# Kernel optimization log

Measured on AMD Instinct MI355X. Metric: run time of the kernel, lower is better.

## Reference

```python
import jax, jax.numpy as jnp
import numpy as np

N, E, D, C = 100000, 640000, 128, 4


def setup_inputs() -> dict:
    key = jax.random.key(0)
    ks = jax.random.split(key, 8)
    s = 1.0 / np.sqrt(D)
    return {
        "x": jax.random.normal(ks[0], (N, D), jnp.float32),
        "edge_index": jax.random.randint(ks[1], (2, E), 0, N),
        "edge_attr": jax.random.normal(ks[2], (E, D), jnp.float32),
        "masks": jax.random.uniform(ks[3], (C, N), jnp.float32),
        "W1": jax.random.normal(ks[4], (C, D, D), jnp.float32) * s,
        "b1": jnp.zeros((C, D), jnp.float32),
        "W2": jax.random.normal(ks[5], (C, D, D), jnp.float32) * s,
        "b2": jnp.zeros((C, D), jnp.float32),
        "eps": jnp.zeros((C,), jnp.float32),
        "gamma": jnp.ones((C, D), jnp.float32),
        "beta": jnp.zeros((C, D), jnp.float32),
        "run_mean": jnp.zeros((C, D), jnp.float32),
        "run_var": jnp.ones((C, D), jnp.float32),
    }


def reference(x, edge_index, edge_attr, masks, W1, b1, W2, b2, eps, gamma, beta, run_mean, run_var):
    BN_EPS = 1e-5
    src, dst = edge_index[0], edge_index[1]
    x_in = x
    for c in range(C):
        # GINEConv: sum_{j->i} relu(x_j + e_ij), then (1+eps)*x_i + agg -> MLP
        msg = jax.nn.relu(x[src] + edge_attr)                      # [E, D]
        agg = jax.ops.segment_sum(msg, dst, num_segments=x.shape[0])
        h = (1.0 + eps[c]) * x + agg
        h = jax.nn.relu(h @ W1[c] + b1[c]) @ W2[c] + b2[c]
        # masked sublayer residual
        x = masks[c][:, None] * h + x
        # BatchNorm1d (eval mode, running stats)
        x = (x - run_mean[c]) * jax.lax.rsqrt(run_var[c] + BN_EPS) * gamma[c] + beta[c]
    # final relu (dropout is identity in eval) + outer residual
    return x_in + jax.nn.relu(x)
```

## Files before the change

### kernel.cpp

```cpp
#include <hip/hip_runtime.h>
#include <cstddef>

#define D 128
#define CHUNK 1024
#define BM 64
#define LDSH 136

typedef __attribute__((ext_vector_type(8))) short s16x8;
typedef __attribute__((ext_vector_type(8))) unsigned short u16x8;
typedef __attribute__((ext_vector_type(4))) float f32x4;
typedef __attribute__((ext_vector_type(2))) float f32x2;

__device__ __forceinline__ unsigned short f2bf(float f) {
  unsigned u = __builtin_bit_cast(unsigned, f);
  u += 0x7FFFu + ((u >> 16) & 1u);
  return (unsigned short)(u >> 16);
}
__device__ __forceinline__ float bf2f(unsigned short h) {
  unsigned u = ((unsigned)h) << 16;
  return __builtin_bit_cast(float, u);
}
__device__ __forceinline__ unsigned f32x4_to_fp8(float4 v) {
  int r = __builtin_amdgcn_cvt_pk_fp8_f32(v.x, v.y, 0, false);
  r = __builtin_amdgcn_cvt_pk_fp8_f32(v.z, v.w, r, true);
  return (unsigned)r;
}
__device__ __forceinline__ void fp8x4_to_f32(unsigned u, float* o) {
  f32x2 lo = __builtin_amdgcn_cvt_pk_f32_fp8((int)u, false);
  f32x2 hi = __builtin_amdgcn_cvt_pk_f32_fp8((int)u, true);
  o[0] = lo[0]; o[1] = lo[1]; o[2] = hi[0]; o[3] = hi[1];
}

__global__ __launch_bounds__(256) void prep_kernel(
    const int* __restrict__ ei, int E, int nbh,
    int* __restrict__ deg,
    const float* __restrict__ W1, const float* __restrict__ W2,
    const float* __restrict__ gamma, const float* __restrict__ beta,
    const float* __restrict__ rmean, const float* __restrict__ rvar,
    unsigned short* __restrict__ wpk,
    float* __restrict__ bnsc, float* __restrict__ bnbb, int C,
    const float* __restrict__ x_in, unsigned short* __restrict__ xbf, long long n8) {
  int b = blockIdx.x;
  if (b < nbh) {
    int e = b * 256 + threadIdx.x;
    if (e < E) atomicAdd(&deg[ei[E + e]], 1);
    return;
  }
  b -= nbh;
  if (b < C) {
    int c = b;
    const float* Ws[2] = {W1 + (size_t)c * D * D, W2 + (size_t)c * D * D};
    unsigned short* base = wpk + (size_t)c * 2 * D * D;
    if (threadIdx.x < D) {
      int col = threadIdx.x;
      float sc = gamma[(size_t)c * D + col] * rsqrtf(rvar[(size_t)c * D + col] + 1e-5f);
      bnsc[(size_t)c * D + col] = sc;
      bnbb[(size_t)c * D + col] = beta[(size_t)c * D + col] - rmean[(size_t)c * D + col] * sc;
    }
    for (int t = threadIdx.x; t < 2048; t += blockDim.x) {
      int ct = t >> 8, ks = (t >> 6) & 3, l = t & 63;
      int col = ct * 16 + (l & 15);
      int krow = ks * 32 + ((l >> 4) & 3) * 8;
      for (int w = 0; w < 2; ++w) {
        unsigned short* dst = base + (size_t)w * D * D;
        const float* W = Ws[w];
        for (int i = 0; i < 8; ++i)
          dst[(size_t)t * 8 + i] = f2bf(W[(size_t)(krow + i) * D + col]);
      }
    }
    return;
  }
  b -= C;
  long long t = (long long)b * 256 + threadIdx.x;
  if (t >= n8) return;
  float4 v0 = reinterpret_cast<const float4*>(x_in)[t * 2];
  float4 v1 = reinterpret_cast<const float4*>(x_in)[t * 2 + 1];
  ushort4 o0, o1;
  o0.x = f2bf(v0.x); o0.y = f2bf(v0.y); o0.z = f2bf(v0.z); o0.w = f2bf(v0.w);
  o1.x = f2bf(v1.x); o1.y = f2bf(v1.y); o1.z = f2bf(v1.z); o1.w = f2bf(v1.w);
  reinterpret_cast<ushort4*>(xbf)[t * 2] = o0;
  reinterpret_cast<ushort4*>(xbf)[t * 2 + 1] = o1;
}

__global__ __launch_bounds__(256) void partial_kernel(const int* __restrict__ deg,
                                                      int* __restrict__ partial, int N) {
  __shared__ int s[256];
  int base = blockIdx.x * CHUNK;
  int sum = 0;
  for (int j = threadIdx.x; j < CHUNK; j += 256) {
    int idx = base + j;
    sum += (idx < N) ? deg[idx] : 0;
  }
  s[threadIdx.x] = sum;
  __syncthreads();
  for (int ofs = 128; ofs > 0; ofs >>= 1) {
    if (threadIdx.x < ofs) s[threadIdx.x] += s[threadIdx.x + ofs];
    __syncthreads();
  }
  if (threadIdx.x == 0) partial[blockIdx.x] = s[0];
}

__global__ __launch_bounds__(1024) void scanpart_kernel(int* partial, int nb) {
  __shared__ int s[1024];
  int tid = threadIdx.x;
  int v = (tid < nb) ? partial[tid] : 0;
  s[tid] = v;
  __syncthreads();
  for (int o = 1; o < 1024; o <<= 1) {
    int t = (tid >= o) ? s[tid - o] : 0;
    __syncthreads();
    s[tid] += t;
    __syncthreads();
  }
  if (tid < nb) partial[tid] = s[tid] - v;
}

__global__ __launch_bounds__(256) void chunkscan_kernel(const int* __restrict__ deg,
                                                        const int* __restrict__ partial,
                                                        int* __restrict__ off, int N) {
  __shared__ int ws[4];
  int base = blockIdx.x * CHUNK;
  int i0 = base + threadIdx.x * 4;
  int d[4];
  int s = 0;
#pragma unroll
  for (int k = 0; k < 4; ++k) {
    d[k] = (i0 + k < N) ? deg[i0 + k] : 0;
    s += d[k];
  }
  int lane = threadIdx.x & 63;
  int incl = s;
  for (int o = 1; o < 64; o <<= 1) {
    int v = __shfl_up(incl, o, 64);
    if (lane >= o) incl += v;
  }
  int wave = threadIdx.x >> 6;
  if (lane == 63) ws[wave] = incl;
  __syncthreads();
  int wofs = 0;
  for (int w = 0; w < wave; ++w) wofs += ws[w];
  int run = partial[blockIdx.x] + wofs + (incl - s);
#pragma unroll
  for (int k = 0; k < 4; ++k) {
    int idx = i0 + k;
    if (idx < N) {
      off[idx] = run;
      run += d[k];
      if (idx == N - 1) off[N] = run;
    }
  }
}

__global__ __launch_bounds__(256) void scatter_conv_kernel(
    const int* __restrict__ ei, const float* __restrict__ ea,
    const int* __restrict__ off, int* __restrict__ cursor,
    int* __restrict__ sperm, unsigned char* __restrict__ eap, int E) {
  int t = blockIdx.x * 256 + threadIdx.x;
  int lane = t & 31;
  int e = t >> 5;
  if (e >= E) return;
  int p = 0;
  if (lane == 0) {
    int dnode = ei[E + e];
    p = off[dnode] + atomicAdd(&cursor[dnode], 1);
    sperm[p] = ei[e];
  }
  p = __shfl(p, 0, 32);
  float4 v = *reinterpret_cast<const float4*>(ea + (size_t)e * D + lane * 4);
  reinterpret_cast<unsigned*>(eap)[(size_t)p * 32 + lane] = f32x4_to_fp8(v);
}

__global__ __launch_bounds__(256, 5) void layer_kernel(
    const unsigned short* __restrict__ xbf,
    const unsigned char* __restrict__ eap,
    const int* __restrict__ off, const int* __restrict__ sperm,
    const float* __restrict__ epsp,
    const unsigned short* __restrict__ wpk,
    const float* __restrict__ b1, const float* __restrict__ b2,
    const float* __restrict__ mask,
    const float* __restrict__ bnsc, const float* __restrict__ bnbb,
    const float* __restrict__ x_in, float* __restrict__ out,
    unsigned short* __restrict__ xbf_out,
    int N, int is_last) {
  __shared__ __align__(16) unsigned short smem[BM * LDSH];
  unsigned short* h_s = smem;
  unsigned short* t_s = smem;
  unsigned short* y_s = smem;

  const int tid = threadIdx.x;
  const int r0 = blockIdx.x * BM;
  const float one_eps = 1.0f + epsp[0];

  {
    const int qw = tid >> 4;
    const int l16 = tid & 15;
#pragma unroll
    for (int it = 0; it < 4; ++it) {
      int row = it * 16 + qw;
      int gr = r0 + row;
      unsigned short* ph = h_s + row * LDSH + l16 * 8;
      if (gr >= N) {
        u16x8 z = {0, 0, 0, 0, 0, 0, 0, 0};
        *reinterpret_cast<u16x8*>(ph) = z;
        continue;
      }
      int beg = off[gr], end = off[gr + 1];
      float acc[8] = {0.f, 0.f, 0.f, 0.f, 0.f, 0.f, 0.f, 0.f};
      for (int i = beg; i < end; i += 8) {
        int n = end - i;
        int idx[8], sidx[8];
#pragma unroll
        for (int k = 0; k < 8; ++k) idx[k] = (k < n) ? i + k : i;
#pragma unroll
        for (int k = 0; k < 8; ++k) sidx[k] = sperm[idx[k]];
        u16x8 xv[8];
        uint2 eu[8];
#pragma unroll
        for (int k = 0; k < 8; ++k) {
          xv[k] = *reinterpret_cast<const u16x8*>(xbf + (size_t)sidx[k] * D + l16 * 8);
          eu[k] = *reinterpret_cast<const uint2*>(eap + (size_t)idx[k] * D + l16 * 8);
        }
#pragma unroll
        for (int k = 0; k < 8; ++k) {
          if (k == 0 || k < n) {
            float ev[8];
            fp8x4_to_f32(eu[k].x, ev);
            fp8x4_to_f32(eu[k].y, ev + 4);
#pragma unroll
            for (int q = 0; q < 8; ++q)
              acc[q] += fmaxf(bf2f((unsigned short)xv[k][q]) + ev[q], 0.f);
          }
        }
      }
      u16x8 xo = *reinterpret_cast<const u16x8*>(xbf + (size_t)gr * D + l16 * 8);
      u16x8 hi8;
#pragma unroll
      for (int q = 0; q < 8; ++q)
        hi8[q] = f2bf(fmaf(one_eps, bf2f((unsigned short)xo[q]), acc[q]));
      *reinterpret_cast<u16x8*>(ph) = hi8;
    }
  }
  __syncthreads();

  const int l = tid & 63;
  const int wave = tid >> 6;
  const int wm = wave >> 1;
  const int wn = wave & 1;
  const int cl = l & 15;
  const int kq = l >> 4;

  f32x4 acc1[2][4];
  {
    s16x8 a[2][4];
#pragma unroll
    for (int rt = 0; rt < 2; ++rt) {
      int row = wm * 32 + rt * 16 + cl;
#pragma unroll
      for (int ks = 0; ks < 4; ++ks)
        a[rt][ks] = *reinterpret_cast<const s16x8*>(h_s + row * LDSH + ks * 32 + kq * 8);
    }
    const s16x8* w1 = reinterpret_cast<const s16x8*>(wpk);
#pragma unroll
    for (int ct = 0; ct < 4; ++ct) {
      int gct = wn * 4 + ct;
      f32x4 a0 = {0.f, 0.f, 0.f, 0.f};
      f32x4 a1 = {0.f, 0.f, 0.f, 0.f};
#pragma unroll
      for (int ks = 0; ks < 4; ++ks) {
        s16x8 bh = w1[(gct * 4 + ks) * 64 + l];
        a0 = __builtin_amdgcn_mfma_f32_16x16x32_bf16(a[0][ks], bh, a0, 0, 0, 0);
        a1 = __builtin_amdgcn_mfma_f32_16x16x32_bf16(a[1][ks], bh, a1, 0, 0, 0);
      }
      acc1[0][ct] = a0;
      acc1[1][ct] = a1;
    }
  }
  __syncthreads();

#pragma unroll
  for (int ct = 0; ct < 4; ++ct) {
    int gct = wn * 4 + ct;
    float bv = b1[gct * 16 + cl];
#pragma unroll
    for (int i = 0; i < 4; ++i) {
      t_s[(wm * 32 + kq * 4 + i) * LDSH + gct * 16 + cl] = f2bf(fmaxf(acc1[0][ct][i] + bv, 0.f));
      t_s[(wm * 32 + 16 + kq * 4 + i) * LDSH + gct * 16 + cl] = f2bf(fmaxf(acc1[1][ct][i] + bv, 0.f));
    }
  }
  __syncthreads();

  f32x4 acc2[2][4];
  {
    s16x8 a[2][4];
#pragma unroll
    for (int rt = 0; rt < 2; ++rt) {
      int row = wm * 32 + rt * 16 + cl;
#pragma unroll
      for (int ks = 0; ks < 4; ++ks)
        a[rt][ks] = *reinterpret_cast<const s16x8*>(t_s + row * LDSH + ks * 32 + kq * 8);
    }
    const s16x8* w2 = reinterpret_cast<const s16x8*>(wpk + D * D);
#pragma unroll
    for (int ct = 0; ct < 4; ++ct) {
      int gct = wn * 4 + ct;
      f32x4 a0 = {0.f, 0.f, 0.f, 0.f};
      f32x4 a1 = {0.f, 0.f, 0.f, 0.f};
#pragma unroll
      for (int ks = 0; ks < 4; ++ks) {
        s16x8 bh = w2[(gct * 4 + ks) * 64 + l];
        a0 = __builtin_amdgcn_mfma_f32_16x16x32_bf16(a[0][ks], bh, a0, 0, 0, 0);
        a1 = __builtin_amdgcn_mfma_f32_16x16x32_bf16(a[1][ks], bh, a1, 0, 0, 0);
      }
      acc2[0][ct] = a0;
      acc2[1][ct] = a1;
    }
  }
  __syncthreads();

#pragma unroll
  for (int ct = 0; ct < 4; ++ct) {
    int gct = wn * 4 + ct;
#pragma unroll
    for (int i = 0; i < 4; ++i) {
      y_s[(wm * 32 + kq * 4 + i) * LDSH + gct * 16 + cl] = f2bf(acc2[0][ct][i]);
      y_s[(wm * 32 + 16 + kq * 4 + i) * LDSH + gct * 16 + cl] = f2bf(acc2[1][ct][i]);
    }
  }
  __syncthreads();

  for (int j = tid; j < BM * 16; j += 256) {
    int row = j >> 4, c8 = j & 15;
    int gr = r0 + row;
    if (gr >= N) continue;
    u16x8 yb = *reinterpret_cast<const u16x8*>(y_s + row * LDSH + c8 * 8);
    u16x8 xr = *reinterpret_cast<const u16x8*>(xbf + (size_t)gr * D + c8 * 8);
    float mk = mask[gr];
    const float* b2p = b2 + c8 * 8;
    const float* scp = bnsc + c8 * 8;
    const float* bbp = bnbb + c8 * 8;
    float4 b20 = *reinterpret_cast<const float4*>(b2p);
    float4 b21 = *reinterpret_cast<const float4*>(b2p + 4);
    float4 sc0 = *reinterpret_cast<const float4*>(scp);
    float4 sc1 = *reinterpret_cast<const float4*>(scp + 4);
    float4 bb0 = *reinterpret_cast<const float4*>(bbp);
    float4 bb1 = *reinterpret_cast<const float4*>(bbp + 4);
    float b2a[8] = {b20.x, b20.y, b20.z, b20.w, b21.x, b21.y, b21.z, b21.w};
    float sca[8] = {sc0.x, sc0.y, sc0.z, sc0.w, sc1.x, sc1.y, sc1.z, sc1.w};
    float bba[8] = {bb0.x, bb0.y, bb0.z, bb0.w, bb1.x, bb1.y, bb1.z, bb1.w};
    float vo[8];
#pragma unroll
    for (int q = 0; q < 8; ++q) {
      float v = fmaf(mk, bf2f((unsigned short)yb[q]) + b2a[q], bf2f((unsigned short)xr[q]));
      vo[q] = fmaf(v, sca[q], bba[q]);
    }
    if (is_last) {
      const float* xip = x_in + (size_t)gr * D + c8 * 8;
      float4 xi0 = *reinterpret_cast<const float4*>(xip);
      float4 xi1 = *reinterpret_cast<const float4*>(xip + 4);
      float xi[8] = {xi0.x, xi0.y, xi0.z, xi0.w, xi1.x, xi1.y, xi1.z, xi1.w};
#pragma unroll
      for (int q = 0; q < 8; ++q) vo[q] = xi[q] + fmaxf(vo[q], 0.f);
      float4 w0 = make_float4(vo[0], vo[1], vo[2], vo[3]);
      float4 w1 = make_float4(vo[4], vo[5], vo[6], vo[7]);
      float* op = out + (size_t)gr * D + c8 * 8;
      *reinterpret_cast<float4*>(op) = w0;
      *reinterpret_cast<float4*>(op + 4) = w1;
    } else {
      u16x8 o;
#pragma unroll
      for (int q = 0; q < 8; ++q) o[q] = f2bf(vo[q]);
      *reinterpret_cast<u16x8*>(xbf_out + (size_t)gr * D + c8 * 8) = o;
    }
  }
}

static inline char* align_up(char* p, size_t a) {
  return (char*)(((size_t)p + a - 1) & ~(a - 1));
}

extern "C" void kernel_launch(void* const* d_in, const int* in_sizes, int n_in,
                              void* d_out, int out_size, void* d_ws, size_t ws_size,
                              hipStream_t stream) {
  const float* x_in  = (const float*)d_in[0];
  const int*   ei    = (const int*)d_in[1];
  const float* ea    = (const float*)d_in[2];
  const float* masks = (const float*)d_in[3];
  const float* W1    = (const float*)d_in[4];
  const float* b1    = (const float*)d_in[5];
  const float* W2    = (const float*)d_in[6];
  const float* b2    = (const float*)d_in[7];
  const float* eps   = (const float*)d_in[8];
  const float* gamma = (const float*)d_in[9];
  const float* beta  = (const float*)d_in[10];
  const float* rmean = (const float*)d_in[11];
  const float* rvar  = (const float*)d_in[12];
  const int N = in_sizes[0] / D;
  const int E = in_sizes[1] / 2;
  const int C = in_sizes[8];
  const int nb = (N + CHUNK - 1) / CHUNK;

  char* w = (char*)d_ws;
  int* deg     = (int*)w;    w += (size_t)N * sizeof(int);
  int* cursor  = (int*)w;    w += (size_t)N * sizeof(int);
  int* off     = (int*)w;    w += (size_t)(N + 1) * sizeof(int);
  int* partial = (int*)w;    w += (size_t)(nb + 1) * sizeof(int);
  int* sperm   = (int*)w;    w += (size_t)E * sizeof(int);
  w = align_up(w, 128);
  unsigned short* xbfA = (unsigned short*)w;  w += (size_t)N * D * sizeof(unsigned short);
  unsigned short* xbfB = (unsigned short*)w;  w += (size_t)N * D * sizeof(unsigned short);
  unsigned short* wpk  = (unsigned short*)w;  w += (size_t)C * 2 * D * D * sizeof(unsigned short);
  float* bnsc = (float*)w;   w += (size_t)C * D * sizeof(float);
  float* bnbb = (float*)w;   w += (size_t)C * D * sizeof(float);
  w = align_up(w, 128);
  unsigned char* eap = (unsigned char*)w;

  hipMemsetAsync(deg, 0, (size_t)2 * N * sizeof(int), stream);
  const int nbh = (E + 255) / 256;
  const long long n8 = (long long)N * D / 8;
  const int nbx = (int)((n8 + 255) / 256);
  prep_kernel<<<nbh + C + nbx, 256, 0, stream>>>(
      ei, E, nbh, deg,
      W1, W2, gamma, beta, rmean, rvar, wpk, bnsc, bnbb, C,
      x_in, xbfA, n8);
  partial_kernel<<<nb, 256, 0, stream>>>(deg, partial, N);
  scanpart_kernel<<<1, 1024, 0, stream>>>(partial, nb);
  chunkscan_kernel<<<nb, 256, 0, stream>>>(deg, partial, off, N);
  scatter_conv_kernel<<<(E + 7) / 8, 256, 0, stream>>>(ei, ea, off, cursor, sperm, eap, E);

  const int blocks = (N + BM - 1) / BM;
  const unsigned short* xbf_cur = xbfA;
  for (int c = 0; c < C; ++c) {
    unsigned short* xbf_next = (xbf_cur == xbfA) ? xbfB : xbfA;
    layer_kernel<<<blocks, 256, 0, stream>>>(
        xbf_cur, eap, off, sperm, eps + c,
        wpk + (size_t)c * 2 * D * D,
        b1 + (size_t)c * D, b2 + (size_t)c * D,
        masks + (size_t)c * N,
        bnsc + (size_t)c * D, bnbb + (size_t)c * D,
        x_in, (float*)d_out, xbf_next, N, (c == C - 1) ? 1 : 0);
    xbf_cur = xbf_next;
  }
}
```

Baseline: 430.9 us.

## Record edge rank during degree count and prefetch neighbor indices across rows

The degree-count atomicAdd now stores each edge's slot rank, so the scatter kernel computes positions directly and no longer needs a second atomic pass or the cursor array. In the layer kernel's gather phase, all row offsets are loaded up front, the first 8 source indices for the next row are prefetched while the current row is processed, and the first 8-edge chunk is issued early. The aim is to hide gather latency and cut atomic traffic. The cost is an extra E-sized rank array, more registers in a kernel launched with an occupancy hint of 5, and duplicated loop code.

```diff
diff --git a/kernel.cpp b/kernel.cpp
--- a/kernel.cpp
+++ b/kernel.cpp
@@ -33,7 +33,7 @@
 
 __global__ __launch_bounds__(256) void prep_kernel(
     const int* __restrict__ ei, int E, int nbh,
-    int* __restrict__ deg,
+    int* __restrict__ deg, int* __restrict__ rank,
     const float* __restrict__ W1, const float* __restrict__ W2,
     const float* __restrict__ gamma, const float* __restrict__ beta,
     const float* __restrict__ rmean, const float* __restrict__ rvar,
@@ -43,7 +43,7 @@
   int b = blockIdx.x;
   if (b < nbh) {
     int e = b * 256 + threadIdx.x;
-    if (e < E) atomicAdd(&deg[ei[E + e]], 1);
+    if (e < E) rank[e] = atomicAdd(&deg[ei[E + e]], 1);
     return;
   }
   b -= nbh;
@@ -153,19 +153,15 @@
 
 __global__ __launch_bounds__(256) void scatter_conv_kernel(
     const int* __restrict__ ei, const float* __restrict__ ea,
-    const int* __restrict__ off, int* __restrict__ cursor,
+    const int* __restrict__ off, const int* __restrict__ rank,
     int* __restrict__ sperm, unsigned char* __restrict__ eap, int E) {
   int t = blockIdx.x * 256 + threadIdx.x;
   int lane = t & 31;
   int e = t >> 5;
   if (e >= E) return;
-  int p = 0;
-  if (lane == 0) {
-    int dnode = ei[E + e];
-    p = off[dnode] + atomicAdd(&cursor[dnode], 1);
-    sperm[p] = ei[e];
-  }
-  p = __shfl(p, 0, 32);
+  int d = ei[E + e];
+  int p = off[d] + rank[e];
+  if (lane == 0) sperm[p] = ei[e];
   float4 v = *reinterpret_cast<const float4*>(ea + (size_t)e * D + lane * 4);
   reinterpret_cast<unsigned*>(eap)[(size_t)p * 32 + lane] = f32x4_to_fp8(v);
 }
@@ -194,35 +190,47 @@
   {
     const int qw = tid >> 4;
     const int l16 = tid & 15;
+    int begs[4], ends[4];
+#pragma unroll
+    for (int it = 0; it < 4; ++it) {
+      int gr = r0 + it * 16 + qw;
+      int g = min(gr, N - 1);
+      begs[it] = off[g];
+      ends[it] = off[g + 1];
+    }
+    int sp[8];
+    {
+      int lim = max(ends[0] - 1, 0);
+#pragma unroll
+      for (int k = 0; k < 8; ++k) sp[k] = sperm[min(begs[0] + k, lim)];
+    }
 #pragma unroll
     for (int it = 0; it < 4; ++it) {
       int row = it * 16 + qw;
       int gr = r0 + row;
-      unsigned short* ph = h_s + row * LDSH + l16 * 8;
-      if (gr >= N) {
-        u16x8 z = {0, 0, 0, 0, 0, 0, 0, 0};
-        *reinterpret_cast<u16x8*>(ph) = z;
-        continue;
-      }
-      int beg = off[gr], end = off[gr + 1];
+      int beg = begs[it], end = ends[it];
+      int n0 = end - beg;
       float acc[8] = {0.f, 0.f, 0.f, 0.f, 0.f, 0.f, 0.f, 0.f};
-      for (int i = beg; i < end; i += 8) {
-        int n = end - i;
-        int idx[8], sidx[8];
-#pragma unroll
-        for (int k = 0; k < 8; ++k) idx[k] = (k < n) ? i + k : i;
-#pragma unroll
-        for (int k = 0; k < 8; ++k) sidx[k] = sperm[idx[k]];
-        u16x8 xv[8];
-        uint2 eu[8];
+      u16x8 xv[8];
+      uint2 eu[8];
+      if (n0 > 0) {
 #pragma unroll
         for (int k = 0; k < 8; ++k) {
-          xv[k] = *reinterpret_cast<const u16x8*>(xbf + (size_t)sidx[k] * D + l16 * 8);
-          eu[k] = *reinterpret_cast<const uint2*>(eap + (size_t)idx[k] * D + l16 * 8);
+          int ik = min(beg + k, end - 1);
+          xv[k] = *reinterpret_cast<const u16x8*>(xbf + (size_t)sp[k] * D + l16 * 8);
+          eu[k] = *reinterpret_cast<const uint2*>(eap + (size_t)ik * D + l16 * 8);
         }
+      }
+      int nsp[8];
+      if (it < 3) {
+        int lim = max(ends[it + 1] - 1, 0);
+#pragma unroll
+        for (int k = 0; k < 8; ++k) nsp[k] = sperm[min(begs[it + 1] + k, lim)];
+      }
+      if (n0 > 0) {
 #pragma unroll
         for (int k = 0; k < 8; ++k) {
-          if (k == 0 || k < n) {
+          if (k == 0 || k < n0) {
             float ev[8];
             fp8x4_to_f32(eu[k].x, ev);
             fp8x4_to_f32(eu[k].y, ev + 4);
@@ -232,12 +240,48 @@
           }
         }
       }
-      u16x8 xo = *reinterpret_cast<const u16x8*>(xbf + (size_t)gr * D + l16 * 8);
-      u16x8 hi8;
-#pragma unroll
-      for (int q = 0; q < 8; ++q)
-        hi8[q] = f2bf(fmaf(one_eps, bf2f((unsigned short)xo[q]), acc[q]));
-      *reinterpret_cast<u16x8*>(ph) = hi8;
+      for (int i = beg + 8; i < end; i += 8) {
+        int n = end - i;
+        int idx[8], sidx[8];
+#pragma unroll
+        for (int k = 0; k < 8; ++k) idx[k] = (k < n) ? i + k : i;
+#pragma unroll
+        for (int k = 0; k < 8; ++k) sidx[k] = sperm[idx[k]];
+        u16x8 txv[8];
+        uint2 teu[8];
+#pragma unroll
+        for (int k = 0; k < 8; ++k) {
+          txv[k] = *reinterpret_cast<const u16x8*>(xbf + (size_t)sidx[k] * D + l16 * 8);
+          teu[k] = *reinterpret_cast<const uint2*>(eap + (size_t)idx[k] * D + l16 * 8);
+        }
+#pragma unroll
+        for (int k = 0; k < 8; ++k) {
+          if (k == 0 || k < n) {
+            float ev[8];
+            fp8x4_to_f32(teu[k].x, ev);
+            fp8x4_to_f32(teu[k].y, ev + 4);
+#pragma unroll
+            for (int q = 0; q < 8; ++q)
+              acc[q] += fmaxf(bf2f((unsigned short)txv[k][q]) + ev[q], 0.f);
+          }
+        }
+      }
+      unsigned short* ph = h_s + row * LDSH + l16 * 8;
+      if (gr < N) {
+        u16x8 xo = *reinterpret_cast<const u16x8*>(xbf + (size_t)gr * D + l16 * 8);
+        u16x8 hi8;
+#pragma unroll
+        for (int q = 0; q < 8; ++q)
+          hi8[q] = f2bf(fmaf(one_eps, bf2f((unsigned short)xo[q]), acc[q]));
+        *reinterpret_cast<u16x8*>(ph) = hi8;
+      } else {
+        u16x8 z = {0, 0, 0, 0, 0, 0, 0, 0};
+        *reinterpret_cast<u16x8*>(ph) = z;
+      }
+      if (it < 3) {
+#pragma unroll
+        for (int k = 0; k < 8; ++k) sp[k] = nsp[k];
+      }
     }
   }
   __syncthreads();
@@ -401,9 +445,9 @@
 
   char* w = (char*)d_ws;
   int* deg     = (int*)w;    w += (size_t)N * sizeof(int);
-  int* cursor  = (int*)w;    w += (size_t)N * sizeof(int);
   int* off     = (int*)w;    w += (size_t)(N + 1) * sizeof(int);
   int* partial = (int*)w;    w += (size_t)(nb + 1) * sizeof(int);
+  int* rank    = (int*)w;    w += (size_t)E * sizeof(int);
   int* sperm   = (int*)w;    w += (size_t)E * sizeof(int);
   w = align_up(w, 128);
   unsigned short* xbfA = (unsigned short*)w;  w += (size_t)N * D * sizeof(unsigned short);
@@ -414,18 +458,18 @@
   w = align_up(w, 128);
   unsigned char* eap = (unsigned char*)w;
 
-  hipMemsetAsync(deg, 0, (size_t)2 * N * sizeof(int), stream);
+  hipMemsetAsync(deg, 0, (size_t)N * sizeof(int), stream);
   const int nbh = (E + 255) / 256;
   const long long n8 = (long long)N * D / 8;
   const int nbx = (int)((n8 + 255) / 256);
   prep_kernel<<<nbh + C + nbx, 256, 0, stream>>>(
-      ei, E, nbh, deg,
+      ei, E, nbh, deg, rank,
       W1, W2, gamma, beta, rmean, rvar, wpk, bnsc, bnbb, C,
       x_in, xbfA, n8);
   partial_kernel<<<nb, 256, 0, stream>>>(deg, partial, N);
   scanpart_kernel<<<1, 1024, 0, stream>>>(partial, nb);
   chunkscan_kernel<<<nb, 256, 0, stream>>>(deg, partial, off, N);
-  scatter_conv_kernel<<<(E + 7) / 8, 256, 0, stream>>>(ei, ea, off, cursor, sperm, eap, E);
+  scatter_conv_kernel<<<(E + 7) / 8, 256, 0, stream>>>(ei, ea, off, rank, sperm, eap, E);
 
   const int blocks = (N + BM - 1) / BM;
   const unsigned short* xbf_cur = xbfA;
```

After: 668.0 us. 55.0% more time.
